# Optimization experiments

Measured on AMD Instinct MI355X. Metric: run time of the kernel, lower is better.

Reference implementation:

```python
import jax, jax.numpy as jnp
import numpy as np

NUM_CLASSES = 10000
EMBED_LEN_DECODER = 100
DECODER_EMBEDDING = 768
DUPLICATE_FACTOR = int(NUM_CLASSES / EMBED_LEN_DECODER + 0.999)  # 100
BATCH = 512


def setup_inputs() -> dict:
    key = jax.random.key(0)
    k_h, k_w = jax.random.split(key)
    h = jax.random.normal(k_h, (BATCH, EMBED_LEN_DECODER, DECODER_EMBEDDING), dtype=jnp.float32)
    # xavier_normal over (decoder_embedding, duplicate_factor) fan dims
    std = (2.0 / (DECODER_EMBEDDING + DUPLICATE_FACTOR)) ** 0.5
    duplicate_pooling = std * jax.random.normal(
        k_w, (EMBED_LEN_DECODER, DECODER_EMBEDDING, DUPLICATE_FACTOR), dtype=jnp.float32)
    bias = jnp.zeros((NUM_CLASSES,), dtype=jnp.float32)
    return {"h": h, "duplicate_pooling": duplicate_pooling, "bias": bias}


def reference(h, duplicate_pooling, bias):
    # per-group batched matmul: out[b, i, f] = sum_d h[b, i, d] * W[i, d, f]
    out_extrap = jnp.einsum('bid,idf->bif', h, duplicate_pooling)
    # flatten groups, truncate to num_classes, add bias
    logits = out_extrap.reshape(h.shape[0], -1)[:, :NUM_CLASSES] + bias
    return logits
```

## Files before the change

### kernel.cpp

```cpp
#include <hip/hip_runtime.h>

typedef __attribute__((ext_vector_type(4))) float f32x4;
typedef __attribute__((ext_vector_type(8))) __bf16 bf16x8;
typedef __attribute__((ext_vector_type(8))) unsigned short ushort8v;
typedef __attribute__((ext_vector_type(4))) unsigned short ushort4v;

#define NGRP  100
#define DDIM  768
#define FDIM  100
#define NCLS  10000
#define KS    64
#define NSTEP 12
#define MBLK  64
#define LDB   72
#define NTILE 7

static __device__ __forceinline__ unsigned short f2bf(float f) {
    __bf16 b = (__bf16)f;
    return __builtin_bit_cast(unsigned short, b);
}

__global__ __launch_bounds__(256, 2) void gfcp_mfma(
    const float* __restrict__ H, const float* __restrict__ W,
    const float* __restrict__ Bv, float* __restrict__ Out)
{
    __shared__ unsigned short Blds[2][112 * LDB];

    const int bid  = blockIdx.x;
    const int wgid = (bid & 7) * 100 + (bid >> 3);
    const int g    = wgid >> 3;
    const int m0   = (wgid & 7) * MBLK;

    const int tid  = threadIdx.x;
    const int lane = tid & 63;
    const int wv   = tid >> 6;
    const int r16  = lane & 15;
    const int kg   = lane >> 4;

    const int kq0 = tid / 25, fq0 = tid % 25;
    const bool has1 = (tid + 256) < 400;
    const int idx1 = tid + 256;
    const int kq1 = idx1 / 25, fq1 = idx1 % 25;

    const float* Wg   = W + (size_t)g * (DDIM * FDIM);
    const float* Arow = H + (size_t)(m0 + wv * 16 + r16) * (NGRP * DDIM)
                          + (size_t)g * DDIM + (size_t)kg * 8;

    f32x4 acc[NTILE];
#pragma unroll
    for (int t = 0; t < NTILE; ++t) acc[t] = (f32x4)(0.0f);

    f32x4 bA[2][4];
    f32x4 bB[8];

    auto loadA = [&](int slot, int k0) {
        const float* p = Arow + k0;
        bA[slot][0] = *(const f32x4*)(p);
        bA[slot][1] = *(const f32x4*)(p + 4);
        bA[slot][2] = *(const f32x4*)(p + 32);
        bA[slot][3] = *(const f32x4*)(p + 36);
    };
    auto loadB = [&](int k0) {
        const float* p0 = Wg + (size_t)(k0 + kq0 * 4) * FDIM + fq0 * 4;
#pragma unroll
        for (int r = 0; r < 4; ++r) bB[r] = *(const f32x4*)(p0 + r * FDIM);
        if (has1) {
            const float* p1 = Wg + (size_t)(k0 + kq1 * 4) * FDIM + fq1 * 4;
#pragma unroll
            for (int r = 0; r < 4; ++r) bB[4 + r] = *(const f32x4*)(p1 + r * FDIM);
        }
    };
    auto writeB = [&](int buf) {
        unsigned short* bl = &Blds[buf][0];
#pragma unroll
        for (int c = 0; c < 4; ++c) {
            ushort4v v;
            v.x = f2bf(bB[0][c]); v.y = f2bf(bB[1][c]);
            v.z = f2bf(bB[2][c]); v.w = f2bf(bB[3][c]);
            *(ushort4v*)(bl + (fq0 * 4 + c) * LDB + kq0 * 4) = v;
        }
        if (has1) {
#pragma unroll
            for (int c = 0; c < 4; ++c) {
                ushort4v v;
                v.x = f2bf(bB[4][c]); v.y = f2bf(bB[5][c]);
                v.z = f2bf(bB[6][c]); v.w = f2bf(bB[7][c]);
                *(ushort4v*)(bl + (fq1 * 4 + c) * LDB + kq1 * 4) = v;
            }
        }
    };
    auto compute = [&](int buf, int slot) {
        const unsigned short* bl = &Blds[buf][0];
#pragma unroll
        for (int s = 0; s < 2; ++s) {
            const f32x4 a0 = bA[slot][s * 2 + 0];
            const f32x4 a1 = bA[slot][s * 2 + 1];
            ushort8v au;
            au[0] = f2bf(a0[0]); au[1] = f2bf(a0[1]); au[2] = f2bf(a0[2]); au[3] = f2bf(a0[3]);
            au[4] = f2bf(a1[0]); au[5] = f2bf(a1[1]); au[6] = f2bf(a1[2]); au[7] = f2bf(a1[3]);
            const bf16x8 af = __builtin_bit_cast(bf16x8, au);
            const int kb = s * 32 + kg * 8;
#pragma unroll
            for (int t = 0; t < NTILE; ++t) {
                const ushort8v bu = *(const ushort8v*)(bl + (t * 16 + r16) * LDB + kb);
                const bf16x8 bf = __builtin_bit_cast(bf16x8, bu);
                acc[t] = __builtin_amdgcn_mfma_f32_16x16x32_bf16(af, bf, acc[t], 0, 0, 0);
            }
        }
    };

    loadB(0);
    loadA(0, 0);
    loadA(1, KS);
    writeB(0);
    loadB(KS);
    __syncthreads();

#pragma unroll
    for (int t = 0; t < NSTEP; ++t) {
        const int cur = t & 1;
        compute(cur, cur);
        if (t + 1 < NSTEP) {
            writeB(cur ^ 1);
            if (t + 2 < NSTEP) {
                loadB((t + 2) * KS);
                loadA(cur, (t + 2) * KS);
            }
            __syncthreads();
        }
    }

    const int orow  = m0 + wv * 16 + kg * 4;
    const int fbase = g * FDIM;
#pragma unroll
    for (int t = 0; t < NTILE; ++t) {
        const int fc = t * 16 + r16;
        if (fc < FDIM) {
            const float bv = Bv[fbase + fc];
#pragma unroll
            for (int r = 0; r < 4; ++r) {
                Out[(size_t)(orow + r) * NCLS + fbase + fc] = acc[t][r] + bv;
            }
        }
    }
}

extern "C" void kernel_launch(void* const* d_in, const int* in_sizes, int n_in,
                              void* d_out, int out_size, void* d_ws, size_t ws_size,
                              hipStream_t stream) {
    const float* H  = (const float*)d_in[0];
    const float* W  = (const float*)d_in[1];
    const float* Bv = (const float*)d_in[2];
    float* Out = (float*)d_out;
    gfcp_mfma<<<dim3(800), dim3(256), 0, stream>>>(H, W, Bv, Out);
}
```

Before: 46.23 us.

## Pre-transpose weights to bf16 in a separate kernel and read B directly from global

Adds a pre-pass kernel that converts W to bf16 and transposes it to [g][f][d] in workspace. The main kernel then drops its LDS double buffer and barriers, loading B fragments straight from global memory (held in L2) into MFMA operands. The cost is an extra launch plus a write and re-read of the converted weights on every call, and B loads now come from global memory rather than shared memory.

After: 105.8 us. 2.29x slower.

```diff
diff --git a/kernel.cpp b/kernel.cpp
--- a/kernel.cpp
+++ b/kernel.cpp
@@ -9,27 +9,55 @@
 #define DDIM  768
 #define FDIM  100
 #define NCLS  10000
-#define KS    64
 #define NSTEP 12
-#define MBLK  64
-#define LDB   72
 #define NTILE 7
+#define WT_G  (FDIM * DDIM)
 
 static __device__ __forceinline__ unsigned short f2bf(float f) {
     __bf16 b = (__bf16)f;
     return __builtin_bit_cast(unsigned short, b);
 }
 
-__global__ __launch_bounds__(256, 2) void gfcp_mfma(
-    const float* __restrict__ H, const float* __restrict__ W,
+__global__ __launch_bounds__(256) void transpose_w(
+    const float* __restrict__ W, unsigned short* __restrict__ Wt)
+{
+    __shared__ unsigned short lds[FDIM * 66];
+    const int b   = blockIdx.x;
+    const int g   = b / 12;
+    const int d0  = (b % 12) * 64;
+    const int tid = threadIdx.x;
+
+    const float* Wg = W + (size_t)g * (DDIM * FDIM) + (size_t)d0 * FDIM;
+#pragma unroll
+    for (int j = 0; j < 25; ++j) {
+        const int i = tid + j * 256;
+        const int r = i / 100, f = i % 100;
+        lds[f * 66 + r] = f2bf(Wg[i]);
+    }
+    __syncthreads();
+
+    unsigned short* Wo = Wt + (size_t)g * WT_G + d0;
+#pragma unroll
+    for (int j = 0; j < 7; ++j) {
+        const int u = tid + j * 256;
+        const int f = u >> 4, kk = (u & 15) * 4;
+        if (f < FDIM) {
+            ushort4v v;
+            v.x = lds[f * 66 + kk + 0]; v.y = lds[f * 66 + kk + 1];
+            v.z = lds[f * 66 + kk + 2]; v.w = lds[f * 66 + kk + 3];
+            *(ushort4v*)(Wo + (size_t)f * DDIM + kk) = v;
+        }
+    }
+}
+
+__global__ __launch_bounds__(256, 2) void gfcp_main(
+    const float* __restrict__ H, const unsigned short* __restrict__ Wt,
     const float* __restrict__ Bv, float* __restrict__ Out)
 {
-    __shared__ unsigned short Blds[2][112 * LDB];
-
     const int bid  = blockIdx.x;
     const int wgid = (bid & 7) * 100 + (bid >> 3);
     const int g    = wgid >> 3;
-    const int m0   = (wgid & 7) * MBLK;
+    const int m0   = (wgid & 7) * 64;
 
     const int tid  = threadIdx.x;
     const int lane = tid & 63;
@@ -37,96 +65,46 @@
     const int r16  = lane & 15;
     const int kg   = lane >> 4;
 
-    const int kq0 = tid / 25, fq0 = tid % 25;
-    const bool has1 = (tid + 256) < 400;
-    const int idx1 = tid + 256;
-    const int kq1 = idx1 / 25, fq1 = idx1 % 25;
+    const int row = m0 + wv * 16 + r16;
+    const float* Ap = H + (size_t)row * (NGRP * DDIM) + (size_t)g * DDIM + kg * 8;
 
-    const float* Wg   = W + (size_t)g * (DDIM * FDIM);
-    const float* Arow = H + (size_t)(m0 + wv * 16 + r16) * (NGRP * DDIM)
-                          + (size_t)g * DDIM + (size_t)kg * 8;
+    const unsigned short* Bbase = Wt + (size_t)g * WT_G + kg * 8;
+    const unsigned short* Bp[NTILE];
+#pragma unroll
+    for (int t = 0; t < NTILE; ++t) {
+        int f = t * 16 + r16;
+        if (f > FDIM - 1) f = FDIM - 1;
+        Bp[t] = Bbase + (size_t)f * DDIM;
+    }
 
     f32x4 acc[NTILE];
 #pragma unroll
     for (int t = 0; t < NTILE; ++t) acc[t] = (f32x4)(0.0f);
 
-    f32x4 bA[2][4];
-    f32x4 bB[8];
-
-    auto loadA = [&](int slot, int k0) {
-        const float* p = Arow + k0;
-        bA[slot][0] = *(const f32x4*)(p);
-        bA[slot][1] = *(const f32x4*)(p + 4);
-        bA[slot][2] = *(const f32x4*)(p + 32);
-        bA[slot][3] = *(const f32x4*)(p + 36);
-    };
-    auto loadB = [&](int k0) {
-        const float* p0 = Wg + (size_t)(k0 + kq0 * 4) * FDIM + fq0 * 4;
 #pragma unroll
-        for (int r = 0; r < 4; ++r) bB[r] = *(const f32x4*)(p0 + r * FDIM);
-        if (has1) {
-            const float* p1 = Wg + (size_t)(k0 + kq1 * 4) * FDIM + fq1 * 4;
-#pragma unroll
-            for (int r = 0; r < 4; ++r) bB[4 + r] = *(const f32x4*)(p1 + r * FDIM);
-        }
-    };
-    auto writeB = [&](int buf) {
-        unsigned short* bl = &Blds[buf][0];
-#pragma unroll
-        for (int c = 0; c < 4; ++c) {
-            ushort4v v;
-            v.x = f2bf(bB[0][c]); v.y = f2bf(bB[1][c]);
-            v.z = f2bf(bB[2][c]); v.w = f2bf(bB[3][c]);
-            *(ushort4v*)(bl + (fq0 * 4 + c) * LDB + kq0 * 4) = v;
-        }
-        if (has1) {
-#pragma unroll
-            for (int c = 0; c < 4; ++c) {
-                ushort4v v;
-                v.x = f2bf(bB[4][c]); v.y = f2bf(bB[5][c]);
-                v.z = f2bf(bB[6][c]); v.w = f2bf(bB[7][c]);
-                *(ushort4v*)(bl + (fq1 * 4 + c) * LDB + kq1 * 4) = v;
-            }
-        }
-    };
-    auto compute = [&](int buf, int slot) {
-        const unsigned short* bl = &Blds[buf][0];
-#pragma unroll
-        for (int s = 0; s < 2; ++s) {
-            const f32x4 a0 = bA[slot][s * 2 + 0];
-            const f32x4 a1 = bA[slot][s * 2 + 1];
-            ushort8v au;
-            au[0] = f2bf(a0[0]); au[1] = f2bf(a0[1]); au[2] = f2bf(a0[2]); au[3] = f2bf(a0[3]);
-            au[4] = f2bf(a1[0]); au[5] = f2bf(a1[1]); au[6] = f2bf(a1[2]); au[7] = f2bf(a1[3]);
-            const bf16x8 af = __builtin_bit_cast(bf16x8, au);
-            const int kb = s * 32 + kg * 8;
-#pragma unroll
-            for (int t = 0; t < NTILE; ++t) {
-                const ushort8v bu = *(const ushort8v*)(bl + (t * 16 + r16) * LDB + kb);
-                const bf16x8 bf = __builtin_bit_cast(bf16x8, bu);
-                acc[t] = __builtin_amdgcn_mfma_f32_16x16x32_bf16(af, bf, acc[t], 0, 0, 0);
-            }
-        }
-    };
-
-    loadB(0);
-    loadA(0, 0);
-    loadA(1, KS);
-    writeB(0);
-    loadB(KS);
-    __syncthreads();
+    for (int step = 0; step < NSTEP; ++step) {
+        const int k0 = step * 64;
+        const f32x4 a0 = *(const f32x4*)(Ap + k0);
+        const f32x4 a1 = *(const f32x4*)(Ap + k0 + 4);
+        const f32x4 a2 = *(const f32x4*)(Ap + k0 + 32);
+        const f32x4 a3 = *(const f32x4*)(Ap + k0 + 36);
+        ushort8v u0, u1;
+        u0[0] = f2bf(a0[0]); u0[1] = f2bf(a0[1]); u0[2] = f2bf(a0[2]); u0[3] = f2bf(a0[3]);
+        u0[4] = f2bf(a1[0]); u0[5] = f2bf(a1[1]); u0[6] = f2bf(a1[2]); u0[7] = f2bf(a1[3]);
+        u1[0] = f2bf(a2[0]); u1[1] = f2bf(a2[1]); u1[2] = f2bf(a2[2]); u1[3] = f2bf(a2[3]);
+        u1[4] = f2bf(a3[0]); u1[5] = f2bf(a3[1]); u1[6] = f2bf(a3[2]); u1[7] = f2bf(a3[3]);
+        const bf16x8 af0 = __builtin_bit_cast(bf16x8, u0);
+        const bf16x8 af1 = __builtin_bit_cast(bf16x8, u1);
 
 #pragma unroll
-    for (int t = 0; t < NSTEP; ++t) {
-        const int cur = t & 1;
-        compute(cur, cur);
-        if (t + 1 < NSTEP) {
-            writeB(cur ^ 1);
-            if (t + 2 < NSTEP) {
-                loadB((t + 2) * KS);
-                loadA(cur, (t + 2) * KS);
-            }
-            __syncthreads();
+        for (int t = 0; t < NTILE; ++t) {
+            const bf16x8 bf = *(const bf16x8*)(Bp[t] + k0);
+            acc[t] = __builtin_amdgcn_mfma_f32_16x16x32_bf16(af0, bf, acc[t], 0, 0, 0);
+        }
+#pragma unroll
+        for (int t = 0; t < NTILE; ++t) {
+            const bf16x8 bf = *(const bf16x8*)(Bp[t] + k0 + 32);
+            acc[t] = __builtin_amdgcn_mfma_f32_16x16x32_bf16(af1, bf, acc[t], 0, 0, 0);
         }
     }
 
@@ -152,5 +130,8 @@
     const float* W  = (const float*)d_in[1];
     const float* Bv = (const float*)d_in[2];
     float* Out = (float*)d_out;
-    gfcp_mfma<<<dim3(800), dim3(256), 0, stream>>>(H, W, Bv, Out);
+    unsigned short* Wt = (unsigned short*)d_ws;
+
+    transpose_w<<<dim3(1200), dim3(256), 0, stream>>>(W, Wt);
+    gfcp_main<<<dim3(800), dim3(256), 0, stream>>>(H, Wt, Bv, Out);
 }
```
